# Kernel tuning notes

Measured on AMD Instinct MI355X. Metric: run time of the kernel, lower is better.

Reference implementation:

```python
import jax, jax.numpy as jnp
import numpy as np

TEMP = 0.07
MAX_SAMPLES = 2048
RADIUS = 10
HARD_FRAC = 0.75
FG_LABEL = 1
B, C, H, W = 8, 64, 256, 256
BLOCK = 32

MAX_FG = MAX_SAMPLES // 2                      # 1024
NEG_BUDGET = MAX_SAMPLES - MAX_FG              # 1024
HARD_BUDGET = int(round(HARD_FRAC * NEG_BUDGET))  # 768
RAND_BUDGET = NEG_BUDGET - HARD_BUDGET         # 256


def setup_inputs() -> dict:
    key = jax.random.key(0)
    feats = jax.random.normal(key, (B, C, H, W), dtype=jnp.float32)
    # 32x32-block checkerboard labels: guarantees abundant fg / ring / interior-bg pools
    ii, jj = jnp.meshgrid(jnp.arange(H), jnp.arange(W), indexing='ij')
    lbl = (((ii // BLOCK) + (jj // BLOCK)) % 2).astype(jnp.int32)
    labels = jnp.broadcast_to(lbl, (B, H, W))
    return {"feats": feats, "labels": labels}


def _forward(feats, labels):
    Bn, Cn, Hn, Wn = feats.shape
    n_pix = Hn * Wn
    f_flat = feats.reshape(Bn, Cn, n_pix).transpose(0, 2, 1)  # [B, P, C]
    l_flat = labels.reshape(Bn, n_pix)

    fg = labels == FG_LABEL                                   # [B, H, W]
    k = 2 * RADIUS + 1
    # max-pool dilation of fg mask (kernel k, stride 1, pad RADIUS == SAME)
    dil = jax.lax.reduce_window(fg.astype(jnp.float32), -jnp.inf, jax.lax.max,
                                (1, k, k), (1, 1, 1), 'SAME') > 0.0
    fg_flat = fg.reshape(Bn, n_pix)
    bg_flat = ~fg_flat                                        # all pixels valid (no ignore)
    ring_flat = dil.reshape(Bn, n_pix) & ~fg_flat & bg_flat
    bgonly_flat = bg_flat & ~ring_flat

    def per_image(f, y, fgm, ringm, bgm, key):
        k1, k2, k3 = jax.random.split(key, 3)
        def pick(mask, kk, n):
            # random subset of n true positions (== randperm[:n] in distribution)
            s = jnp.where(mask, jax.random.uniform(kk, mask.shape), -1.0)
            return jax.lax.top_k(s, n)[1]
        idx = jnp.concatenate([pick(fgm, k1, MAX_FG),
                               pick(ringm, k2, HARD_BUDGET),
                               pick(bgm, k3, RAND_BUDGET)])    # [K]
        fs = f[idx]                                            # [K, C]
        ys = y[idx]
        fs = fs / jnp.maximum(jnp.linalg.norm(fs, axis=1, keepdims=True), 1e-12)
        logits = fs @ fs.T / TEMP                              # [K, K]
        logits = logits - jax.lax.stop_gradient(logits.max(axis=1, keepdims=True))
        eye = jnp.eye(MAX_SAMPLES, dtype=bool)
        pos = (ys[:, None] == ys[None, :]) & ~eye
        exp_l = jnp.exp(logits) * (~eye)
        denom = jnp.maximum(exp_l.sum(axis=1), 1e-8)
        pos_sum = jnp.maximum(jnp.where(pos, exp_l, 0.0).sum(axis=1), 1e-8)
        valid = pos.any(axis=1) & (ys == FG_LABEL)
        loss_terms = -jnp.log(pos_sum / denom)
        n_valid = jnp.maximum(valid.sum(), 1)
        return jnp.where(valid, loss_terms, 0.0).sum() / n_valid

    keys = jax.random.split(jax.random.key(1), Bn)
    losses = jax.vmap(per_image)(f_flat, l_flat, fg_flat, ring_flat, bgonly_flat, keys)
    return losses.mean()


def reference(feats, labels):
    return _forward(feats, labels)
```

## Files before the change

kernel.cpp:

```cpp
#include <hip/hip_runtime.h>
#include <stdint.h>

#define NPIX   65536
#define NIMG   8
#define NCH    64
#define KSEL   2048
#define NFG    1024
#define NRING  768
#define NBG    256
#define INV_TEMP 14.285714285714286f

typedef __attribute__((ext_vector_type(8))) short bf16x8;
typedef __attribute__((ext_vector_type(4))) float f32x4;

__device__ __forceinline__ void tf2x32(uint32_t k0, uint32_t k1,
                                       uint32_t& x0, uint32_t& x1) {
  const uint32_t ks2 = k0 ^ k1 ^ 0x1BD11BDAu;
  x0 += k0; x1 += k1;
#define TF_RND(r) { x0 += x1; x1 = (x1 << (r)) | (x1 >> (32 - (r))); x1 ^= x0; }
  TF_RND(13) TF_RND(15) TF_RND(26) TF_RND(6)
  x0 += k1;  x1 += ks2 + 1u;
  TF_RND(17) TF_RND(29) TF_RND(16) TF_RND(24)
  x0 += ks2; x1 += k0 + 2u;
  TF_RND(13) TF_RND(15) TF_RND(26) TF_RND(6)
  x0 += k0;  x1 += k1 + 3u;
  TF_RND(17) TF_RND(29) TF_RND(16) TF_RND(24)
  x0 += k1;  x1 += ks2 + 4u;
  TF_RND(13) TF_RND(15) TF_RND(26) TF_RND(6)
  x0 += ks2; x1 += k0 + 5u;
#undef TF_RND
}

__device__ __forceinline__ ushort f2bf(float f) {
  uint32_t u = __float_as_uint(f);
  return (ushort)((u + 0x7FFFu + ((u >> 16) & 1u)) >> 16);
}

__global__ __launch_bounds__(256) void prep_hash(const int* __restrict__ labels,
                                                 uint32_t* __restrict__ mgrp,
                                                 uint32_t* __restrict__ hist32,
                                                 float* __restrict__ out) {
  __shared__ uint64_t fgs[112], hds[112], fgb[32], dlb[32];
  __shared__ uint32_t lh[768];
  __shared__ uint32_t skeys[6];
  const int tid = threadIdx.x;
  const int img = blockIdx.x >> 5;
  const int band = blockIdx.x & 31;

  if (blockIdx.x == 0 && tid == 0) out[0] = 0.0f;

  if (tid < 3) {
    uint32_t kb0 = 0u, kb1 = (uint32_t)img;
    tf2x32(0u, 1u, kb0, kb1);
    uint32_t x0 = 0u, x1 = (uint32_t)tid;
    tf2x32(kb0, kb1, x0, x1);
    skeys[tid * 2 + 0] = x0;
    skeys[tid * 2 + 1] = x1;
  }
  for (int t = tid; t < 768; t += 256) lh[t] = 0;

  const int rbase = band * 8 - 10;
  for (int it = 0; it < 28; ++it) {
    int hr = rbase + it;
    bool bit = false;
    if (hr >= 0 && hr < 256) bit = (labels[(img << 16) + (hr << 8) + tid] == 1);
    uint64_t m = __ballot(bit);
    if ((tid & 63) == 0) fgs[it * 4 + (tid >> 6)] = m;
  }
  __syncthreads();

  for (int w = tid; w < 112; w += 256) {
    int wc = w & 3;
    uint64_t x = fgs[w];
    uint64_t L = wc > 0 ? fgs[w - 1] : 0ull;
    uint64_t R = wc < 3 ? fgs[w + 1] : 0ull;
    uint64_t acc = x;
    #pragma unroll
    for (int s = 1; s <= 10; ++s) {
      acc |= (x << s) | (L >> (64 - s));
      acc |= (x >> s) | (R << (64 - s));
    }
    hds[w] = acc;
  }
  __syncthreads();

  for (int w = tid; w < 32; w += 256) {
    int r = w >> 2, wc = w & 3;
    uint64_t acc = 0ull;
    #pragma unroll
    for (int dr = 0; dr <= 20; ++dr) acc |= hds[(r + dr) * 4 + wc];
    fgb[w] = fgs[(r + 10) * 4 + wc];
    dlb[w] = acc;
  }
  __syncthreads();

  const uint32_t K00 = skeys[0], K01 = skeys[1];
  const uint32_t K10 = skeys[2], K11 = skeys[3];
  const uint32_t K20 = skeys[4], K21 = skeys[5];
  const int pbase = blockIdx.x * 2048;

  #pragma unroll
  for (int k = 0; k < 8; ++k) {
    int off = k * 256 + tid;
    int pix = (pbase + off) & 65535;
    int lw = off >> 6, bp = off & 63;
    uint32_t fgbit = (uint32_t)((fgb[lw] >> bp) & 1ull);
    uint32_t dilbit = (uint32_t)((dlb[lw] >> bp) & 1ull);
    uint32_t grp = fgbit ? 0u : (dilbit ? 1u : 2u);
    uint32_t k0 = grp == 0 ? K00 : grp == 1 ? K10 : K20;
    uint32_t k1 = grp == 0 ? K01 : grp == 1 ? K11 : K21;
    uint32_t x0 = 0u, x1 = (uint32_t)pix;
    tf2x32(k0, k1, x0, x1);
    uint32_t m = (x0 ^ x1) >> 9;
    mgrp[pbase + off] = (m << 2) | grp;
    atomicAdd(&lh[grp * 256 + (m >> 15)], 1u);
  }
  __syncthreads();
  for (int t = tid; t < 768; t += 256) hist32[blockIdx.x * 768 + t] = lh[t];
}

__global__ __launch_bounds__(256) void topk_emit(const uint32_t* __restrict__ mgrp,
                                                 const uint32_t* __restrict__ hist32,
                                                 uint32_t* __restrict__ TG,
                                                 uint32_t* __restrict__ candcnt,
                                                 unsigned long long* __restrict__ cand,
                                                 int* __restrict__ idx_out) {
  __shared__ uint32_t hh[768];
  __shared__ uint32_t sT[3];
  __shared__ uint32_t cA[3][32], cB[3][32];
  __shared__ uint32_t preA[3], preB[3];
  __shared__ uint32_t runA[3], runB[3];
  __shared__ uint32_t wcA[3][4], wcB[3][4];
  const int tid = threadIdx.x;
  const int b = blockIdx.x >> 5;
  const int band = blockIdx.x & 31;
  const int base = blockIdx.x * 2048;

  uint32_t vv[8];
  #pragma unroll
  for (int k = 0; k < 8; ++k) vv[k] = mgrp[base + k * 256 + tid];

  for (int t = tid; t < 768; t += 256) {
    uint32_t s = 0;
    const uint32_t* hp = hist32 + (size_t)b * 24576 + t;
    #pragma unroll
    for (int bd = 0; bd < 32; ++bd) s += hp[bd * 768];
    hh[t] = s;
  }
  __syncthreads();

  if (tid < 3) {
    uint32_t nsel = tid == 0 ? NFG : tid == 1 ? NRING : NBG;
    const uint32_t* h = hh + tid * 256;
    uint32_t cum = 0; int T = 255;
    for (; T > 0; --T) {
      uint32_t c = h[T];
      if (cum + c >= nsel) break;
      cum += c;
    }
    sT[tid] = (uint32_t)T;
    runA[tid] = 0; runB[tid] = 0;
    if (band == 0) {
      TG[(b * 3 + tid) * 2] = (uint32_t)T;
      TG[(b * 3 + tid) * 2 + 1] = cum;
      candcnt[b * 3 + tid] = h[T];
    }
  }
  __syncthreads();
  const uint32_t T0 = sT[0], T1 = sT[1], T2 = sT[2];

  if (tid < 96) {
    int g = tid >> 5, bd = tid & 31;
    uint32_t T = g == 0 ? T0 : g == 1 ? T1 : T2;
    const uint32_t* hp = hist32 + (size_t)b * 24576 + bd * 768 + g * 256;
    uint32_t sA = 0;
    for (int t = (int)T + 1; t < 256; ++t) sA += hp[t];
    cA[g][bd] = sA;
    cB[g][bd] = hp[T];
  }
  __syncthreads();
  if (tid < 3) {
    uint32_t pa = 0, pb = 0;
    for (int bd = 0; bd < band; ++bd) { pa += cA[tid][bd]; pb += cB[tid][bd]; }
    preA[tid] = pa; preB[tid] = pb;
  }
  __syncthreads();

  const int lane = tid & 63, w = tid >> 6;
  #pragma unroll 1
  for (int k = 0; k < 8; ++k) {
    const uint32_t v = vv[k];
    const uint32_t g = v & 3u, bin = v >> 17;
    const uint32_t T = g == 0 ? T0 : g == 1 ? T1 : T2;
    const bool selA = bin > T;
    const bool selB = bin == T;
    const uint64_t mA0 = __ballot(selA && g == 0);
    const uint64_t mA1 = __ballot(selA && g == 1);
    const uint64_t mA2 = __ballot(selA && g == 2);
    const uint64_t mB0 = __ballot(selB && g == 0);
    const uint64_t mB1 = __ballot(selB && g == 1);
    const uint64_t mB2 = __ballot(selB && g == 2);
    if (lane == 0) {
      wcA[0][w] = (uint32_t)__popcll(mA0);
      wcA[1][w] = (uint32_t)__popcll(mA1);
      wcA[2][w] = (uint32_t)__popcll(mA2);
      wcB[0][w] = (uint32_t)__popcll(mB0);
      wcB[1][w] = (uint32_t)__popcll(mB1);
      wcB[2][w] = (uint32_t)__popcll(mB2);
    }
    __syncthreads();
    if (selA || selB) {
      const uint64_t mask = g == 0 ? (selA ? mA0 : mB0)
                          : g == 1 ? (selA ? mA1 : mB1)
                                   : (selA ? mA2 : mB2);
      const uint32_t intra = (uint32_t)__popcll(mask & ((1ull << lane) - 1ull));
      uint32_t wbase = 0;
      for (int w2 = 0; w2 < w; ++w2) wbase += selA ? wcA[g][w2] : wcB[g][w2];
      const int pix = (base + k * 256 + tid) & 65535;
      if (selA) {
        const uint32_t slot = preA[g] + runA[g] + wbase + intra;
        const int seg = g == 0 ? 0 : g == 1 ? NFG : (NFG + NRING);
        idx_out[b * KSEL + seg + (int)slot] = pix;
      } else {
        const uint32_t c = preB[g] + runB[g] + wbase + intra;
        if (c < 1024u) {
          const uint32_t m = v >> 2;
          cand[((size_t)b * 3 + g) * 1024 + c] =
              ((unsigned long long)m << 16) | (uint32_t)pix;
        }
      }
    }
    __syncthreads();
    if (tid < 3) {
      runA[tid] += wcA[tid][0] + wcA[tid][1] + wcA[tid][2] + wcA[tid][3];
      runB[tid] += wcB[tid][0] + wcB[tid][1] + wcB[tid][2] + wcB[tid][3];
    }
    __syncthreads();
  }
}

#define GA 16
__global__ __launch_bounds__(256) void gather_rank_t(
    const float* __restrict__ feats, const int* __restrict__ idx,
    const uint32_t* __restrict__ TG, const uint32_t* __restrict__ candcnt,
    const unsigned long long* __restrict__ cand, ushort* __restrict__ fs) {
  __shared__ float tile[GA * 65];
  __shared__ float ssb[16 * GA];
  __shared__ float sscale[GA];
  __shared__ int lidx[GA];
  __shared__ unsigned long long cb[1024];
  const int tid = threadIdx.x;
  const int img = blockIdx.x >> 7;
  const int win = (blockIdx.x & 127) * GA;
  int seg, segoff, nsel;
  if (win < NFG)               { seg = 0; segoff = 0;            nsel = NFG; }
  else if (win < NFG + NRING)  { seg = 1; segoff = NFG;          nsel = NRING; }
  else                         { seg = 2; segoff = NFG + NRING;  nsel = NBG; }
  const int task = img * 3 + seg;
  const uint32_t G = TG[task * 2 + 1];
  const int poslo = win - segoff;

  if (tid < GA) {
    if ((uint32_t)(poslo + tid) < G)
      lidx[tid] = idx[img * KSEL + win + tid];
  }
  const bool needRank = (uint32_t)(poslo + GA) > G;
  if (needRank) {
    const int c = (int)(candcnt[task] < 1024u ? candcnt[task] : 1024u);
    const int r = nsel - (int)G;
    for (int i = tid; i < c; i += 256) cb[i] = cand[task * 1024 + i];
    __syncthreads();
    for (int i = tid; i < c; i += 256) {
      unsigned long long me = cb[i];
      uint32_t mm = (uint32_t)(me >> 16), pi = (uint32_t)(me & 0xFFFFu);
      int rank = 0;
      for (int j = 0; j < c; ++j) {
        unsigned long long o = cb[j];
        uint32_t om = (uint32_t)(o >> 16), op = (uint32_t)(o & 0xFFFFu);
        if (om > mm || (om == mm && op < pi)) ++rank;
      }
      if (rank < r) {
        int slot = (int)G + rank - poslo;
        if (slot >= 0 && slot < GA) lidx[slot] = (int)pi;
      }
    }
  }
  __syncthreads();

  const int a = tid & 15, q = tid >> 4;
  const int pix = lidx[a];
  const float* fb = feats + ((size_t)img * NCH + q * 4) * NPIX + pix;
  float ss = 0.f;
  #pragma unroll
  for (int k = 0; k < 4; ++k) {
    float v = fb[(size_t)k * NPIX];
    tile[a * 65 + q * 4 + k] = v;
    ss += v * v;
  }
  ssb[q * GA + a] = ss;
  __syncthreads();
  if (q == 0) {
    float tot = 0.f;
    #pragma unroll
    for (int q2 = 0; q2 < 16; ++q2) tot += ssb[q2 * GA + a];
    sscale[a] = 1.0f / fmaxf(sqrtf(tot), 1e-12f);
  }
  __syncthreads();

  const int row = tid >> 4, c4 = tid & 15;
  const float sc = sscale[row];
  ushort4 v4;
  v4.x = f2bf(tile[row * 65 + c4 * 4 + 0] * sc);
  v4.y = f2bf(tile[row * 65 + c4 * 4 + 1] * sc);
  v4.z = f2bf(tile[row * 65 + c4 * 4 + 2] * sc);
  v4.w = f2bf(tile[row * 65 + c4 * 4 + 3] * sc);
  ((ushort4*)(fs + ((size_t)img * KSEL + win + row) * NCH))[c4] = v4;
}

__global__ __launch_bounds__(1024) void loss_mfma(const ushort* __restrict__ fs,
                                                  float* __restrict__ out) {
  const int img = blockIdx.x & 7;
  const int a0 = (blockIdx.x >> 3) * 32;
  const ushort* X = fs + (size_t)img * KSEL * NCH;
  const int tid = threadIdx.x;
  const int lane = tid & 63, wave = tid >> 6;
  const int quad = lane >> 4, col = lane & 15;
  const int rt = wave >> 3, cseg = wave & 7;

  __shared__ float redD[2][8][16];
  __shared__ float redP[2][4][16];

  const int arow = a0 + rt * 16 + col;
  const bf16x8* Ap = (const bf16x8*)(X + (size_t)arow * NCH + quad * 8);
  const bf16x8 a_lo = Ap[0];
  const bf16x8 a_hi = Ap[4];

  float pD[4] = {0.f, 0.f, 0.f, 0.f};
  float pP[4] = {0.f, 0.f, 0.f, 0.f};
  const int ct0 = cseg * 16;
  const int mbase = a0 + rt * 16 + quad * 4;

  for (int ct = ct0; ct < ct0 + 16; ++ct) {
    const int j = ct * 16 + col;
    const bf16x8* Bp = (const bf16x8*)(X + (size_t)j * NCH + quad * 8);
    bf16x8 b_lo = Bp[0];
    bf16x8 b_hi = Bp[4];
    f32x4 d = {0.f, 0.f, 0.f, 0.f};
    d = __builtin_amdgcn_mfma_f32_16x16x32_bf16(a_lo, b_lo, d, 0, 0, 0);
    d = __builtin_amdgcn_mfma_f32_16x16x32_bf16(a_hi, b_hi, d, 0, 0, 0);
    #pragma unroll
    for (int r = 0; r < 4; ++r) {
      float e = __expf(d[r] * INV_TEMP);
      if (j == mbase + r) e = 0.f;
      pD[r] += e;
      if (cseg < 4) pP[r] += e;
    }
  }

  #pragma unroll
  for (int o = 1; o < 16; o <<= 1) {
    #pragma unroll
    for (int r = 0; r < 4; ++r) {
      pD[r] += __shfl_xor(pD[r], o);
      pP[r] += __shfl_xor(pP[r], o);
    }
  }
  if (col == 0) {
    #pragma unroll
    for (int r = 0; r < 4; ++r) {
      redD[rt][cseg][quad * 4 + r] = pD[r];
      if (cseg < 4) redP[rt][cseg][quad * 4 + r] = pP[r];
    }
  }
  __syncthreads();

  float term = 0.f;
  if (tid < 32) {
    int lrt = tid >> 4, lr = tid & 15;
    float dsum = 0.f, psum = 0.f;
    #pragma unroll
    for (int cs = 0; cs < 8; ++cs) dsum += redD[lrt][cs][lr];
    #pragma unroll
    for (int cs = 0; cs < 4; ++cs) psum += redP[lrt][cs][lr];
    dsum = fmaxf(dsum, 1e-8f);
    psum = fmaxf(psum, 1e-8f);
    term = __logf(dsum) - __logf(psum);
  }
  if (tid < 64) {
    #pragma unroll
    for (int o = 32; o > 0; o >>= 1) term += __shfl_xor(term, o);
    if (tid == 0) atomicAdd(out, term * (1.0f / (NFG * NIMG)));
  }
}

extern "C" void kernel_launch(void* const* d_in, const int* in_sizes, int n_in,
                              void* d_out, int out_size, void* d_ws, size_t ws_size,
                              hipStream_t stream) {
  const float* feats = (const float*)d_in[0];
  const int* labels  = (const int*)d_in[1];
  float* out = (float*)d_out;

  char* ws = (char*)d_ws;
  uint32_t* TG      = (uint32_t*)(ws);
  uint32_t* candcnt = (uint32_t*)(ws + 4096);
  unsigned long long* cand = (unsigned long long*)(ws + 8192);
  int*      idx     = (int*)(ws + 262144);
  uint32_t* mgrp    = (uint32_t*)(ws + 2097152);
  uint32_t* hist32  = (uint32_t*)(ws + 4194304);
  ushort*   fs      = (ushort*)(ws + 8388608);

  hipLaunchKernelGGL(prep_hash, dim3(NIMG * 32), dim3(256), 0, stream,
                     labels, mgrp, hist32, out);
  hipLaunchKernelGGL(topk_emit, dim3(NIMG * 32), dim3(256), 0, stream,
                     mgrp, hist32, TG, candcnt, cand, idx);
  hipLaunchKernelGGL(gather_rank_t, dim3((NIMG * KSEL) / GA), dim3(256), 0, stream,
                     feats, idx, TG, candcnt, cand, fs);
  hipLaunchKernelGGL(loss_mfma, dim3(NIMG * (NFG / 32)), dim3(1024), 0, stream,
                     fs, out);
}
```

Measured before the change: 235.0 us.

## Split gather into per-channel-plane gather and separate normalize kernel

Replaces the per-16-sample gather (one block per 16 samples reading all 64 channel planes) with a per-(image, channel) gather where each block resolves all 2048 sampled indices and reads only one feature plane. This keeps each block's scattered reads within a single 256 KB plane for better cache locality. A new norm_write kernel then computes L2 norms and writes bf16 rows. The cost is that every block repeats the tie-rank resolution for all three segments, plus an extra launch and an fp32 intermediate round trip through global memory.

```diff
diff --git a/kernel.cpp b/kernel.cpp
--- a/kernel.cpp
+++ b/kernel.cpp
@@ -239,36 +239,28 @@
   }
 }
 
-#define GA 16
-__global__ __launch_bounds__(256) void gather_rank_t(
+__global__ __launch_bounds__(256) void gather_stream(
     const float* __restrict__ feats, const int* __restrict__ idx,
     const uint32_t* __restrict__ TG, const uint32_t* __restrict__ candcnt,
-    const unsigned long long* __restrict__ cand, ushort* __restrict__ fs) {
-  __shared__ float tile[GA * 65];
-  __shared__ float ssb[16 * GA];
-  __shared__ float sscale[GA];
-  __shared__ int lidx[GA];
+    const unsigned long long* __restrict__ cand, float* __restrict__ ft) {
+  __shared__ int lpix[KSEL];
   __shared__ unsigned long long cb[1024];
   const int tid = threadIdx.x;
-  const int img = blockIdx.x >> 7;
-  const int win = (blockIdx.x & 127) * GA;
-  int seg, segoff, nsel;
-  if (win < NFG)               { seg = 0; segoff = 0;            nsel = NFG; }
-  else if (win < NFG + NRING)  { seg = 1; segoff = NFG;          nsel = NRING; }
-  else                         { seg = 2; segoff = NFG + NRING;  nsel = NBG; }
-  const int task = img * 3 + seg;
-  const uint32_t G = TG[task * 2 + 1];
-  const int poslo = win - segoff;
-
-  if (tid < GA) {
-    if ((uint32_t)(poslo + tid) < G)
-      lidx[tid] = idx[img * KSEL + win + tid];
-  }
-  const bool needRank = (uint32_t)(poslo + GA) > G;
-  if (needRank) {
+  const int img = blockIdx.x & 7;
+  const int ch  = blockIdx.x >> 3;
+
+  for (int s = tid; s < KSEL; s += 256) lpix[s] = idx[img * KSEL + s];
+  __syncthreads();
+
+  #pragma unroll 1
+  for (int g = 0; g < 3; ++g) {
+    const int segoff = g == 0 ? 0 : g == 1 ? NFG : NFG + NRING;
+    const int nsel   = g == 0 ? NFG : g == 1 ? NRING : NBG;
+    const int task = img * 3 + g;
+    const int G = (int)TG[task * 2 + 1];
+    const int r = nsel - G;
     const int c = (int)(candcnt[task] < 1024u ? candcnt[task] : 1024u);
-    const int r = nsel - (int)G;
-    for (int i = tid; i < c; i += 256) cb[i] = cand[task * 1024 + i];
+    for (int i = tid; i < c; i += 256) cb[i] = cand[(size_t)task * 1024 + i];
     __syncthreads();
     for (int i = tid; i < c; i += 256) {
       unsigned long long me = cb[i];
@@ -279,42 +271,54 @@
         uint32_t om = (uint32_t)(o >> 16), op = (uint32_t)(o & 0xFFFFu);
         if (om > mm || (om == mm && op < pi)) ++rank;
       }
-      if (rank < r) {
-        int slot = (int)G + rank - poslo;
-        if (slot >= 0 && slot < GA) lidx[slot] = (int)pi;
-      }
-    }
-  }
-  __syncthreads();
-
-  const int a = tid & 15, q = tid >> 4;
-  const int pix = lidx[a];
-  const float* fb = feats + ((size_t)img * NCH + q * 4) * NPIX + pix;
-  float ss = 0.f;
-  #pragma unroll
-  for (int k = 0; k < 4; ++k) {
-    float v = fb[(size_t)k * NPIX];
-    tile[a * 65 + q * 4 + k] = v;
-    ss += v * v;
-  }
-  ssb[q * GA + a] = ss;
-  __syncthreads();
-  if (q == 0) {
-    float tot = 0.f;
-    #pragma unroll
-    for (int q2 = 0; q2 < 16; ++q2) tot += ssb[q2 * GA + a];
-    sscale[a] = 1.0f / fmaxf(sqrtf(tot), 1e-12f);
-  }
-  __syncthreads();
-
-  const int row = tid >> 4, c4 = tid & 15;
-  const float sc = sscale[row];
-  ushort4 v4;
-  v4.x = f2bf(tile[row * 65 + c4 * 4 + 0] * sc);
-  v4.y = f2bf(tile[row * 65 + c4 * 4 + 1] * sc);
-  v4.z = f2bf(tile[row * 65 + c4 * 4 + 2] * sc);
-  v4.w = f2bf(tile[row * 65 + c4 * 4 + 3] * sc);
-  ((ushort4*)(fs + ((size_t)img * KSEL + win + row) * NCH))[c4] = v4;
+      if (rank < r) lpix[segoff + G + rank] = (int)pi;
+    }
+    __syncthreads();
+  }
+
+  const float* plane = feats + ((size_t)img * NCH + ch) * NPIX;
+  float* fto = ft + ((size_t)img * NCH + ch) * KSEL;
+  int p[8];
+  #pragma unroll
+  for (int k = 0; k < 8; ++k) p[k] = lpix[k * 256 + tid];
+  float v[8];
+  #pragma unroll
+  for (int k = 0; k < 8; ++k) v[k] = plane[p[k]];
+  #pragma unroll
+  for (int k = 0; k < 8; ++k) fto[k * 256 + tid] = v[k];
+}
+
+__global__ __launch_bounds__(128) void norm_write(const float* __restrict__ ft,
+                                                  ushort* __restrict__ fs) {
+  const int tid = threadIdx.x;
+  const int img = blockIdx.x & 7;
+  const int tile = blockIdx.x >> 3;
+  const int s = tile * 128 + tid;
+  const float* fb = ft + (size_t)img * NCH * KSEL + s;
+  float v[64];
+  float tot = 0.f;
+  #pragma unroll
+  for (int q = 0; q < 16; ++q) {
+    float ss = 0.f;
+    #pragma unroll
+    for (int k = 0; k < 4; ++k) {
+      float x = fb[(size_t)(q * 4 + k) * KSEL];
+      v[q * 4 + k] = x;
+      ss += x * x;
+    }
+    tot += ss;
+  }
+  const float sc = 1.0f / fmaxf(sqrtf(tot), 1e-12f);
+  ushort* row = fs + ((size_t)img * KSEL + s) * NCH;
+  #pragma unroll
+  for (int c4 = 0; c4 < 16; ++c4) {
+    ushort4 o4;
+    o4.x = f2bf(v[c4 * 4 + 0] * sc);
+    o4.y = f2bf(v[c4 * 4 + 1] * sc);
+    o4.z = f2bf(v[c4 * 4 + 2] * sc);
+    o4.w = f2bf(v[c4 * 4 + 3] * sc);
+    ((ushort4*)row)[c4] = o4;
+  }
 }
 
 __global__ __launch_bounds__(1024) void loss_mfma(const ushort* __restrict__ fs,
@@ -407,14 +411,17 @@
   int*      idx     = (int*)(ws + 262144);
   uint32_t* mgrp    = (uint32_t*)(ws + 2097152);
   uint32_t* hist32  = (uint32_t*)(ws + 4194304);
-  ushort*   fs      = (ushort*)(ws + 8388608);
+  float*    ft      = (float*)(ws + 8388608);
+  ushort*   fs      = (ushort*)(ws + 12582912);
 
   hipLaunchKernelGGL(prep_hash, dim3(NIMG * 32), dim3(256), 0, stream,
                      labels, mgrp, hist32, out);
   hipLaunchKernelGGL(topk_emit, dim3(NIMG * 32), dim3(256), 0, stream,
                      mgrp, hist32, TG, candcnt, cand, idx);
-  hipLaunchKernelGGL(gather_rank_t, dim3((NIMG * KSEL) / GA), dim3(256), 0, stream,
-                     feats, idx, TG, candcnt, cand, fs);
+  hipLaunchKernelGGL(gather_stream, dim3(NIMG * NCH), dim3(256), 0, stream,
+                     feats, idx, TG, candcnt, cand, ft);
+  hipLaunchKernelGGL(norm_write, dim3(NIMG * 16), dim3(128), 0, stream,
+                     ft, fs);
   hipLaunchKernelGGL(loss_mfma, dim3(NIMG * (NFG / 32)), dim3(1024), 0, stream,
                      fs, out);
 }
```

After: 259.0 us. +10.2%, slower.
